# Optimization experiments

Measured on AMD Instinct MI355X. Metric: run time of the kernel, lower is better.

## Reference

```python
import math
import jax, jax.numpy as jnp
import numpy as np

B, T, D = 2, 2048, 2048
DH, NQ, NKV = 128, 16, 4
QPG = NQ // NKV  # queries per group = 4
ROPE_BASE = 10000.0
YARN_SCALE = 2.0
ORIG_MAX_LEN = 4096
BETA_FAST, BETA_SLOW = 32.0, 1.0
EPS = 1.1920929e-07  # torch.finfo(float32).eps, RMSNorm default
MSCALE = 0.1 * math.log(YARN_SCALE) + 1.0
ATTN_SCALE = 1.0 / (MSCALE * math.sqrt(DH))


def _yarn_inv_freq():
    inv_freq = 1.0 / ROPE_BASE ** (np.arange(0, DH, 2, dtype=np.float32) / DH)
    wavelengths = 2.0 * math.pi / inv_freq
    low_w = ORIG_MAX_LEN / BETA_SLOW
    high_w = ORIG_MAX_LEN / BETA_FAST
    gamma = np.clip((low_w - wavelengths) / (low_w - high_w), 0.0, 1.0)
    return (gamma * inv_freq + (1.0 - gamma) * inv_freq / YARN_SCALE).astype(np.float32)


def setup_inputs() -> dict:
    key = jax.random.key(0)
    k0, k1, k2, k3 = jax.random.split(key, 4)
    x = jax.random.normal(k0, (B, T, D), jnp.float32)
    Wq = jax.random.normal(k1, (D, DH * NQ), jnp.float32) * 0.02
    Wkv = jax.random.normal(k2, (D, 2 * DH * NKV), jnp.float32) * 0.02
    Wout = jax.random.normal(k3, (DH * NQ, D), jnp.float32) * 0.02
    q_norm_w = jnp.ones((DH,), jnp.float32)
    k_norm_w = jnp.ones((DH,), jnp.float32)
    inv_freq = jnp.asarray(_yarn_inv_freq())
    return {"x": x, "Wq": Wq, "Wkv": Wkv, "Wout": Wout,
            "q_norm_w": q_norm_w, "k_norm_w": k_norm_w, "inv_freq": inv_freq}


def _rmsnorm(x, w):
    ms = jnp.mean(jnp.square(x), axis=-1, keepdims=True)
    return x * jax.lax.rsqrt(ms + EPS) * w


def _apply_rope(x, inv_freq):
    # x: (..., T, DH)
    t = jnp.arange(x.shape[-2], dtype=inv_freq.dtype)
    freqs = jnp.outer(t, inv_freq)               # (T, DH//2)
    emb = jnp.concatenate([freqs, freqs], -1)     # (T, DH)
    cos, sin = jnp.cos(emb), jnp.sin(emb)
    half = x.shape[-1] // 2
    x_rot = jnp.concatenate([-x[..., half:], x[..., :half]], -1)
    return x * cos + x_rot * sin


def reference(x, Wq, Wkv, Wout, q_norm_w, k_norm_w, inv_freq):
    q = x @ Wq                                    # (B, T, NQ*DH)
    kv = x @ Wkv                                  # (B, T, 2*NKV*DH)
    k, v = jnp.split(kv, 2, axis=-1)              # each (B, T, NKV*DH)
    # b t (qpg g d) -> b qpg g t d
    q = q.reshape(B, T, QPG, NKV, DH).transpose(0, 2, 3, 1, 4)
    # b t (g d) -> b g t d
    k = k.reshape(B, T, NKV, DH).transpose(0, 2, 1, 3)
    v = v.reshape(B, T, NKV, DH).transpose(0, 2, 1, 3)
    q = _apply_rope(_rmsnorm(q, q_norm_w), inv_freq)
    k = _apply_rope(_rmsnorm(k, k_norm_w), inv_freq)
    scores = jnp.einsum('bqgtd,bgsd->bqgts', q, k) * ATTN_SCALE
    causal = jnp.tril(jnp.ones((T, T), bool))
    scores = jnp.where(causal, scores, -jnp.inf)
    attn = jax.nn.softmax(scores, axis=-1)
    out = jnp.einsum('bqgts,bgsd->bqgtd', attn, v)
    # b qpg g t d -> b t (qpg g d)
    out = out.transpose(0, 3, 1, 2, 4).reshape(B, T, NQ * DH)
    return out @ Wout
```

## Files before the change

kernel.cpp:

```cpp
#include <hip/hip_runtime.h>
#include <math.h>


typedef __attribute__((ext_vector_type(8))) short s16x8;
typedef __attribute__((ext_vector_type(4))) float f32x4;
typedef __attribute__((ext_vector_type(4))) unsigned int u32x4;

__device__ __forceinline__ unsigned short f2bf(float x) {
  union { float f; unsigned int u; } v; v.f = x;
  return (unsigned short)((v.u + 0x7FFFu + ((v.u >> 16) & 1u)) >> 16);
}

__device__ __forceinline__ float bf2f(unsigned short x) {
  union { unsigned int u; float f; } v; v.u = (unsigned int)x << 16;
  return v.f;
}

__device__ __forceinline__ unsigned int cvt_pk_bf16(float lo, float hi) {
  unsigned int r;
  asm("v_cvt_pk_bf16_f32 %0, %1, %2" : "=v"(r) : "v"(lo), "v"(hi));
  return r;
}

#define GLD_LDS16(g, l)                                            \
  __builtin_amdgcn_global_load_lds(                                \
      (const __attribute__((address_space(1))) void*)(g),          \
      (__attribute__((address_space(3))) void*)(l), 16, 0, 0)

__global__ __launch_bounds__(256) void cast_bf16_k(const float* __restrict__ in,
                                                   unsigned short* __restrict__ out) {
  int i = blockIdx.x * 256 + threadIdx.x;
  float4 v = ((const float4*)in)[i];
  unsigned long long pack = (unsigned long long)f2bf(v.x)
                          | ((unsigned long long)f2bf(v.y) << 16)
                          | ((unsigned long long)f2bf(v.z) << 32)
                          | ((unsigned long long)f2bf(v.w) << 48);
  ((unsigned long long*)out)[i] = pack;
}

__global__ __launch_bounds__(256) void wtrans_k(const float* __restrict__ in,
                                                unsigned short* __restrict__ out,
                                                int R, int C) {
  __shared__ unsigned short lt[64][65];
  const int r0 = blockIdx.x * 64, c0 = blockIdx.y * 64;
  const int j = threadIdx.x & 63, i4 = threadIdx.x >> 6;
#pragma unroll
  for (int p = 0; p < 16; ++p) {
    int i = p * 4 + i4;
    lt[i][j] = f2bf(in[(size_t)(r0 + i) * C + c0 + j]);
  }
  __syncthreads();
#pragma unroll
  for (int p = 0; p < 16; ++p) {
    int i = p * 4 + i4;
    out[(size_t)(c0 + i) * R + r0 + j] = lt[j][i];
  }
}

__global__ __launch_bounds__(256) void trig_k(const float* __restrict__ invf,
                                              float2* __restrict__ cstab) {
  int i = blockIdx.x * 256 + threadIdx.x;
  int t = i >> 6, f = i & 63;
  float s, c;
  sincosf((float)t * invf[f], &s, &c);
  cstab[i] = make_float2(c, s);
}

template <int OUTBF>
__global__ __launch_bounds__(256) void gemm_bt_t(const unsigned short* __restrict__ A,
                                                 const unsigned short* __restrict__ Bt,
                                                 void* __restrict__ Cv,
                                                 int M, int N, int K) {
  __shared__ alignas(16) unsigned short sA[2][128][32];
  __shared__ alignas(16) unsigned short sB[2][128][32];
  const int tid = threadIdx.x;
  const int lane = tid & 63;
  const int w = tid >> 6;
  const int wm = (w >> 1) * 64, wn = (w & 1) * 64;
  const int nwg = gridDim.x * gridDim.y;
  int bid = blockIdx.y * gridDim.x + blockIdx.x;
  bid = (bid & 7) * (nwg >> 3) + (bid >> 3);
  const int m0 = (bid % gridDim.x) * 128, n0 = (bid / gridDim.x) * 128;
  const int l15 = lane & 15, lhi = lane >> 4;
  f32x4 acc[4][4];
#pragma unroll
  for (int i = 0; i < 4; ++i)
#pragma unroll
    for (int j = 0; j < 4; ++j) acc[i][j] = (f32x4){0.f, 0.f, 0.f, 0.f};
  const int row = tid >> 2;
  const int srcslot = (tid & 3) ^ ((row >> 1) & 3);
  const unsigned short* gA0 = A + (size_t)(m0 + row) * K + srcslot * 8;
  const unsigned short* gA1 = A + (size_t)(m0 + 64 + row) * K + srcslot * 8;
  const unsigned short* gB0 = Bt + (size_t)(n0 + row) * K + srcslot * 8;
  const unsigned short* gB1 = Bt + (size_t)(n0 + 64 + row) * K + srcslot * 8;
  char* ldsA = (char*)&sA[0][0][0] + w * 1024;
  char* ldsB = (char*)&sB[0][0][0] + w * 1024;
  auto STAGE = [&](int bb, int k0) {
    GLD_LDS16(gA0 + k0, ldsA + bb * 8192);
    GLD_LDS16(gA1 + k0, ldsA + bb * 8192 + 4096);
    GLD_LDS16(gB0 + k0, ldsB + bb * 8192);
    GLD_LDS16(gB1 + k0, ldsB + bb * 8192 + 4096);
  };
  const int sphys = (lhi ^ ((l15 >> 1) & 3)) * 8;
  const int nt = K >> 5;
  STAGE(0, 0);
  __syncthreads();
  int cur = 0;
  for (int t = 0; t < nt; ++t) {
    if (t + 1 < nt) STAGE(cur ^ 1, (t + 1) * 32);
    s16x8 af[4], bfr[4];
#pragma unroll
    for (int i = 0; i < 4; ++i) af[i] = *(const s16x8*)&sA[cur][wm + i * 16 + l15][sphys];
#pragma unroll
    for (int j = 0; j < 4; ++j) bfr[j] = *(const s16x8*)&sB[cur][wn + j * 16 + l15][sphys];
#pragma unroll
    for (int i = 0; i < 4; ++i)
#pragma unroll
      for (int j = 0; j < 4; ++j)
        acc[i][j] = __builtin_amdgcn_mfma_f32_16x16x32_bf16(af[i], bfr[j], acc[i][j], 0, 0, 0);
    __syncthreads();
    cur ^= 1;
  }
  const int col0 = n0 + wn + l15;
  const int row00 = m0 + wm + lhi * 4;
  if (OUTBF) {
    unsigned short* C = (unsigned short*)Cv;
#pragma unroll
    for (int i = 0; i < 4; ++i)
#pragma unroll
      for (int j = 0; j < 4; ++j)
#pragma unroll
        for (int r = 0; r < 4; ++r)
          C[(size_t)(row00 + i * 16 + r) * N + col0 + j * 16] = f2bf(acc[i][j][r]);
  } else {
    float* C = (float*)Cv;
#pragma unroll
    for (int i = 0; i < 4; ++i)
#pragma unroll
      for (int j = 0; j < 4; ++j)
#pragma unroll
        for (int r = 0; r < 4; ++r)
          C[(size_t)(row00 + i * 16 + r) * N + col0 + j * 16] = acc[i][j][r];
  }
}

__global__ __launch_bounds__(256) void normrope_k(const unsigned short* __restrict__ qkvb,
                                                  const float* __restrict__ qw,
                                                  const float* __restrict__ kw,
                                                  const float2* __restrict__ cstab,
                                                  unsigned short* __restrict__ qT,
                                                  unsigned short* __restrict__ kT) {
  constexpr float FOLD =
      (float)(1.4426950408889634 / ((0.1 * 0.6931471805599453 + 1.0) * 11.313708498984761));
  int wid = blockIdx.x * 4 + (threadIdx.x >> 6);
  int lane = threadIdx.x & 63;
  const unsigned short* src; const float* wgt; unsigned short* dst;
  int t; float fold;
  if (wid < 65536) {
    int bt = wid >> 4, h = wid & 15;
    int b = bt >> 11; t = bt & 2047;
    src = qkvb + (size_t)bt * 3072 + h * 128;
    wgt = qw;
    dst = qT + ((size_t)(b * 16 + h) * 2048 + t) * 128;
    fold = FOLD;
  } else {
    int id = wid - 65536;
    int bt = id >> 2, g = id & 3;
    int b = bt >> 11; t = bt & 2047;
    src = qkvb + (size_t)bt * 3072 + 2048 + g * 128;
    wgt = kw;
    dst = kT + ((size_t)(b * 4 + g) * 2048 + t) * 128;
    fold = 1.0f;
  }
  unsigned int vv = ((const unsigned int*)src)[lane];
  float vx = bf2f((unsigned short)(vv & 0xffff));
  float vy = bf2f((unsigned short)(vv >> 16));
  float ss = vx * vx + vy * vy;
#pragma unroll
  for (int m = 32; m; m >>= 1) ss += __shfl_xor(ss, m);
  float rs = rsqrtf(ss * (1.0f / 128.0f) + 1.1920929e-07f);
  float2 wv = ((const float2*)wgt)[lane];
  float xn0 = vx * rs * wv.x;
  float xn1 = vy * rs * wv.y;
  float px = __shfl_xor(xn0, 32);
  float py = __shfl_xor(xn1, 32);
  float sgn = (lane < 32) ? -1.0f : 1.0f;
  int f0 = (2 * lane) & 63;
  float4 cs = ((const float4*)cstab)[((size_t)t * 64 + f0) >> 1];
  float r0 = (xn0 * cs.x + sgn * px * cs.y) * fold;
  float r1 = (xn1 * cs.z + sgn * py * cs.w) * fold;
  unsigned int packed = (unsigned int)f2bf(r0) | ((unsigned int)f2bf(r1) << 16);
  ((unsigned int*)dst)[lane] = packed;
}

__global__ __launch_bounds__(256) void vtrans_k(const unsigned short* __restrict__ qkvb,
                                                unsigned short* __restrict__ vT) {
  __shared__ unsigned short lt[64][65];
  const int tt0 = blockIdx.x * 64;
  const int dd0 = blockIdx.y * 64;
  const int b = blockIdx.z >> 2, g = blockIdx.z & 3;
  const int j = threadIdx.x & 63, i4 = threadIdx.x >> 6;
  const unsigned short* src = qkvb + (size_t)b * 2048 * 3072 + 2560 + g * 128 + dd0;
#pragma unroll
  for (int p = 0; p < 16; ++p) {
    int i = p * 4 + i4;
    lt[i][j] = src[(size_t)(tt0 + i) * 3072 + j];
  }
  __syncthreads();
  unsigned short* dst = vT + ((size_t)(b * 4 + g) * 128 + dd0) * 2048 + tt0;
  const int jp = (j & 32) | (((j & 15) >> 2) << 3) | (((j >> 4) & 1) << 2) | (j & 3);
#pragma unroll
  for (int p = 0; p < 16; ++p) {
    int d = p * 4 + i4;
    dst[(size_t)d * 2048 + jp] = lt[j][d];
  }
}

__global__ __launch_bounds__(256) void attn_k(const unsigned short* __restrict__ qT,
                                              const unsigned short* __restrict__ kT,
                                              const unsigned short* __restrict__ vT,
                                              unsigned short* __restrict__ ao) {
  __shared__ alignas(16) unsigned short sK[64][136];
  __shared__ alignas(16) unsigned short sVt[128][72];
  const int tid = threadIdx.x;
  const int lane = tid & 63;
  const int w = tid >> 6;
  const int l15 = lane & 15, lhi = lane >> 4;
  const int bid = blockIdx.x;
  const int xg = bid & 7;
  const int b = xg >> 2, g = xg & 3;
  const int hh = (bid >> 3) & 3;
  const int h = hh * 4 + g;
  const int qt = 31 - (bid >> 5);
  const int q0 = qt * 64;
  const unsigned short* Qb = qT + ((size_t)(b * 16 + h) * 2048) * 128;
  const unsigned short* Kb = kT + ((size_t)(b * 4 + g) * 2048) * 128;
  const unsigned short* Vb = vT + ((size_t)(b * 4 + g) * 128) * 2048;
  const int kr = tid >> 4, kc = (tid & 15) * 8;
  const int vr = tid >> 3, vc = (tid & 7) * 8;

  s16x8 qfr[4];
#pragma unroll
  for (int ks = 0; ks < 4; ++ks)
    qfr[ks] = *(const s16x8*)(Qb + (size_t)(q0 + w * 16 + l15) * 128 + ks * 32 + lhi * 8);

  u32x4 gk[4], gv[4];
#pragma unroll
  for (int p = 0; p < 4; ++p) {
    gk[p] = *(const u32x4*)(Kb + (size_t)(p * 16 + kr) * 128 + kc);
    gv[p] = *(const u32x4*)(Vb + (size_t)(p * 32 + vr) * 2048 + vc);
  }
  f32x4 o[8];
#pragma unroll
  for (int i = 0; i < 8; ++i) o[i] = (f32x4){0.f, 0.f, 0.f, 0.f};
  f32x4 o9 = (f32x4){0.f, 0.f, 0.f, 0.f};
  float m_run = -INFINITY;
  s16x8 ones;
#pragma unroll
  for (int j = 0; j < 8; ++j) ones[j] = (short)0x3F80;

  for (int kt = 0; kt <= qt; ++kt) {
    __syncthreads();
#pragma unroll
    for (int p = 0; p < 4; ++p) {
      *(u32x4*)&sK[p * 16 + kr][kc] = gk[p];
      *(u32x4*)&sVt[p * 32 + vr][vc] = gv[p];
    }
    __syncthreads();
    if (kt < qt) {
#pragma unroll
      for (int p = 0; p < 4; ++p) {
        gk[p] = *(const u32x4*)(Kb + (size_t)((kt + 1) * 64 + p * 16 + kr) * 128 + kc);
        gv[p] = *(const u32x4*)(Vb + (size_t)(p * 32 + vr) * 2048 + (kt + 1) * 64 + vc);
      }
    }
    f32x4 s[4];
#pragma unroll
    for (int jn = 0; jn < 4; ++jn) s[jn] = (f32x4){0.f, 0.f, 0.f, 0.f};
#pragma unroll
    for (int ks = 0; ks < 4; ++ks)
#pragma unroll
      for (int jn = 0; jn < 4; ++jn) {
        s16x8 ak = *(const s16x8*)&sK[jn * 16 + l15][ks * 32 + lhi * 8];
        s[jn] = __builtin_amdgcn_mfma_f32_16x16x32_bf16(ak, qfr[ks], s[jn], 0, 0, 0);
      }
    if (kt == qt) {
#pragma unroll
      for (int jn = 0; jn < 4; ++jn)
#pragma unroll
        for (int r = 0; r < 4; ++r)
          if (jn * 16 + lhi * 4 + r > w * 16 + l15) s[jn][r] = -INFINITY;
    }
    float mx = fmaxf(fmaxf(fmaxf(s[0][0], s[0][1]), fmaxf(s[0][2], s[0][3])),
                     fmaxf(fmaxf(s[1][0], s[1][1]), fmaxf(s[1][2], s[1][3])));
    mx = fmaxf(mx, fmaxf(fmaxf(fmaxf(s[2][0], s[2][1]), fmaxf(s[2][2], s[2][3])),
                         fmaxf(fmaxf(s[3][0], s[3][1]), fmaxf(s[3][2], s[3][3]))));
    mx = fmaxf(mx, __shfl_xor(mx, 16));
    mx = fmaxf(mx, __shfl_xor(mx, 32));
    if (!__all(mx - m_run <= 8.0f)) {
      float mnew = fmaxf(m_run, mx);
      float scale = exp2f(m_run - mnew);
      m_run = mnew;
      float sc_o[4];
#pragma unroll
      for (int r = 0; r < 4; ++r) sc_o[r] = __shfl(scale, lhi * 4 + r);
#pragma unroll
      for (int nt = 0; nt < 8; ++nt)
#pragma unroll
        for (int r = 0; r < 4; ++r) o[nt][r] *= sc_o[r];
#pragma unroll
      for (int r = 0; r < 4; ++r) o9[r] *= sc_o[r];
    }
    float pp[4][4];
#pragma unroll
    for (int jn = 0; jn < 4; ++jn)
#pragma unroll
      for (int r = 0; r < 4; ++r) pp[jn][r] = exp2f(s[jn][r] - m_run);
    union { s16x8 v; unsigned int d[4]; } pa0, pa1;
#pragma unroll
    for (int d = 0; d < 2; ++d) {
      pa0.d[d]     = cvt_pk_bf16(pp[0][2 * d], pp[0][2 * d + 1]);
      pa0.d[2 + d] = cvt_pk_bf16(pp[1][2 * d], pp[1][2 * d + 1]);
      pa1.d[d]     = cvt_pk_bf16(pp[2][2 * d], pp[2][2 * d + 1]);
      pa1.d[2 + d] = cvt_pk_bf16(pp[3][2 * d], pp[3][2 * d + 1]);
    }
    o9 = __builtin_amdgcn_mfma_f32_16x16x32_bf16(pa0.v, ones, o9, 0, 0, 0);
    o9 = __builtin_amdgcn_mfma_f32_16x16x32_bf16(pa1.v, ones, o9, 0, 0, 0);
#pragma unroll
    for (int nt = 0; nt < 8; ++nt) {
      s16x8 vb0 = *(const s16x8*)&sVt[nt * 16 + l15][lhi * 8];
      o[nt] = __builtin_amdgcn_mfma_f32_16x16x32_bf16(pa0.v, vb0, o[nt], 0, 0, 0);
    }
#pragma unroll
    for (int nt = 0; nt < 8; ++nt) {
      s16x8 vb1 = *(const s16x8*)&sVt[nt * 16 + l15][32 + lhi * 8];
      o[nt] = __builtin_amdgcn_mfma_f32_16x16x32_bf16(pa1.v, vb1, o[nt], 0, 0, 0);
    }
  }
#pragma unroll
  for (int r = 0; r < 4; ++r) {
    float invr = 1.0f / o9[r];
    int t = q0 + w * 16 + lhi * 4 + r;
    size_t base = ((size_t)b * 2048 + t) * 2048 + h * 128;
#pragma unroll
    for (int nt = 0; nt < 8; ++nt)
      ao[base + nt * 16 + l15] = f2bf(o[nt][r] * invr);
  }
}

extern "C" void kernel_launch(void* const* d_in, const int* in_sizes, int n_in,
                              void* d_out, int out_size, void* d_ws, size_t ws_size,
                              hipStream_t stream) {
  (void)in_sizes; (void)n_in; (void)out_size; (void)ws_size;
  const float* x    = (const float*)d_in[0];
  const float* Wq   = (const float*)d_in[1];
  const float* Wkv  = (const float*)d_in[2];
  const float* Wout = (const float*)d_in[3];
  const float* qw   = (const float*)d_in[4];
  const float* kw   = (const float*)d_in[5];
  const float* invf = (const float*)d_in[6];
  float* out = (float*)d_out;

  char* ws = (char*)d_ws;
  size_t off = 0;
  auto alloc = [&](size_t bytes) -> void* {
    void* p = ws + off; off += (bytes + 255) & ~(size_t)255; return p;
  };
  unsigned short* xb    = (unsigned short*)alloc((size_t)4096 * 2048 * 2);
  unsigned short* wqkvt = (unsigned short*)alloc((size_t)3072 * 2048 * 2);
  unsigned short* wot   = (unsigned short*)alloc((size_t)2048 * 2048 * 2);
  unsigned short* qkvb  = (unsigned short*)alloc((size_t)4096 * 3072 * 2);
  float2* cstab = (float2*)alloc((size_t)2048 * 64 * 8);
  unsigned short* qT = (unsigned short*)alloc((size_t)2 * 16 * 2048 * 128 * 2);
  unsigned short* kT = (unsigned short*)alloc((size_t)2 * 4 * 2048 * 128 * 2);
  unsigned short* vT = (unsigned short*)alloc((size_t)2 * 4 * 128 * 2048 * 2);
  unsigned short* ao = (unsigned short*)alloc((size_t)4096 * 2048 * 2);

  cast_bf16_k<<<8192, 256, 0, stream>>>(x, xb);
  wtrans_k<<<dim3(32, 32), 256, 0, stream>>>(Wq, wqkvt, 2048, 2048);
  wtrans_k<<<dim3(32, 16), 256, 0, stream>>>(Wkv, wqkvt + (size_t)2048 * 2048, 2048, 1024);
  wtrans_k<<<dim3(32, 32), 256, 0, stream>>>(Wout, wot, 2048, 2048);
  trig_k<<<512, 256, 0, stream>>>(invf, cstab);
  gemm_bt_t<1><<<dim3(32, 24), 256, 0, stream>>>(xb, wqkvt, qkvb, 4096, 3072, 2048);
  normrope_k<<<20480, 256, 0, stream>>>(qkvb, qw, kw, cstab, qT, kT);
  vtrans_k<<<dim3(32, 2, 8), 256, 0, stream>>>(qkvb, vT);
  attn_k<<<1024, 256, 0, stream>>>(qT, kT, vT, ao);
  gemm_bt_t<0><<<dim3(32, 16), 256, 0, stream>>>(ao, wot, out, 4096, 2048, 2048);
}
```

Baseline: 222.0 us.

## Use 128x256 tiles with 512 threads and triple-buffered async LDS pipeline in GEMMs

Both projection GEMMs now use a 128x256 output tile computed by 8 waves, with a three-stage LDS ring filled by direct global-to-LDS loads. A vmcnt wait plus a single barrier per K step replaces the two syncthreads, and loads run two stages ahead. MFMA issue is wrapped in raised wave priority. This aims to hide global-load latency and reuse each A tile across twice as many columns, at the cost of more LDS per block and fewer blocks in the grid.

```diff
diff --git a/kernel.cpp b/kernel.cpp
--- a/kernel.cpp
+++ b/kernel.cpp
@@ -67,62 +67,66 @@
 }
 
 template <int OUTBF>
-__global__ __launch_bounds__(256) void gemm_bt_t(const unsigned short* __restrict__ A,
-                                                 const unsigned short* __restrict__ Bt,
-                                                 void* __restrict__ Cv,
-                                                 int M, int N, int K) {
-  __shared__ alignas(16) unsigned short sA[2][128][32];
-  __shared__ alignas(16) unsigned short sB[2][128][32];
+__global__ __launch_bounds__(512) void gemm_bt2_t(const unsigned short* __restrict__ A,
+                                                  const unsigned short* __restrict__ Bt,
+                                                  void* __restrict__ Cv,
+                                                  int M, int N, int K) {
+  __shared__ alignas(16) unsigned short sA[3][128][32];
+  __shared__ alignas(16) unsigned short sB[3][256][32];
   const int tid = threadIdx.x;
   const int lane = tid & 63;
   const int w = tid >> 6;
-  const int wm = (w >> 1) * 64, wn = (w & 1) * 64;
+  const int wm2 = w >> 2, wn4 = w & 3;
+  const int l15 = lane & 15, lhi = lane >> 4;
   const int nwg = gridDim.x * gridDim.y;
   int bid = blockIdx.y * gridDim.x + blockIdx.x;
   bid = (bid & 7) * (nwg >> 3) + (bid >> 3);
-  const int m0 = (bid % gridDim.x) * 128, n0 = (bid / gridDim.x) * 128;
-  const int l15 = lane & 15, lhi = lane >> 4;
+  const int m0 = (bid % gridDim.x) * 128, n0 = (bid / gridDim.x) * 256;
   f32x4 acc[4][4];
 #pragma unroll
   for (int i = 0; i < 4; ++i)
 #pragma unroll
     for (int j = 0; j < 4; ++j) acc[i][j] = (f32x4){0.f, 0.f, 0.f, 0.f};
   const int row = tid >> 2;
-  const int srcslot = (tid & 3) ^ ((row >> 1) & 3);
-  const unsigned short* gA0 = A + (size_t)(m0 + row) * K + srcslot * 8;
-  const unsigned short* gA1 = A + (size_t)(m0 + 64 + row) * K + srcslot * 8;
+  const int srcslot = (tid & 3) ^ ((tid >> 3) & 3);
+  const unsigned short* gA  = A  + (size_t)(m0 + row) * K + srcslot * 8;
   const unsigned short* gB0 = Bt + (size_t)(n0 + row) * K + srcslot * 8;
-  const unsigned short* gB1 = Bt + (size_t)(n0 + 64 + row) * K + srcslot * 8;
+  const unsigned short* gB1 = Bt + (size_t)(n0 + 128 + row) * K + srcslot * 8;
   char* ldsA = (char*)&sA[0][0][0] + w * 1024;
   char* ldsB = (char*)&sB[0][0][0] + w * 1024;
   auto STAGE = [&](int bb, int k0) {
-    GLD_LDS16(gA0 + k0, ldsA + bb * 8192);
-    GLD_LDS16(gA1 + k0, ldsA + bb * 8192 + 4096);
-    GLD_LDS16(gB0 + k0, ldsB + bb * 8192);
-    GLD_LDS16(gB1 + k0, ldsB + bb * 8192 + 4096);
+    GLD_LDS16(gA + k0, ldsA + bb * 8192);
+    GLD_LDS16(gB0 + k0, ldsB + bb * 16384);
+    GLD_LDS16(gB1 + k0, ldsB + bb * 16384 + 8192);
   };
   const int sphys = (lhi ^ ((l15 >> 1) & 3)) * 8;
   const int nt = K >> 5;
   STAGE(0, 0);
-  __syncthreads();
-  int cur = 0;
+  STAGE(1, 32);
   for (int t = 0; t < nt; ++t) {
-    if (t + 1 < nt) STAGE(cur ^ 1, (t + 1) * 32);
-    s16x8 af[4], bfr[4];
-#pragma unroll
-    for (int i = 0; i < 4; ++i) af[i] = *(const s16x8*)&sA[cur][wm + i * 16 + l15][sphys];
-#pragma unroll
-    for (int j = 0; j < 4; ++j) bfr[j] = *(const s16x8*)&sB[cur][wn + j * 16 + l15][sphys];
+    if (t < nt - 1) asm volatile("s_waitcnt vmcnt(3)" ::: "memory");
+    else            asm volatile("s_waitcnt vmcnt(0)" ::: "memory");
+    __builtin_amdgcn_s_barrier();
+    asm volatile("" ::: "memory");
+    if (t + 2 < nt) STAGE((t + 2) % 3, (t + 2) * 32);
+    const int cb = t % 3;
+    s16x8 af[4], bf[4];
 #pragma unroll
     for (int i = 0; i < 4; ++i)
+      af[i] = *(const s16x8*)&sA[cb][wm2 * 64 + i * 16 + l15][sphys];
+#pragma unroll
+    for (int j = 0; j < 4; ++j)
+      bf[j] = *(const s16x8*)&sB[cb][wn4 * 64 + j * 16 + l15][sphys];
+    __builtin_amdgcn_s_setprio(1);
+#pragma unroll
+    for (int i = 0; i < 4; ++i)
 #pragma unroll
       for (int j = 0; j < 4; ++j)
-        acc[i][j] = __builtin_amdgcn_mfma_f32_16x16x32_bf16(af[i], bfr[j], acc[i][j], 0, 0, 0);
-    __syncthreads();
-    cur ^= 1;
-  }
-  const int col0 = n0 + wn + l15;
-  const int row00 = m0 + wm + lhi * 4;
+        acc[i][j] = __builtin_amdgcn_mfma_f32_16x16x32_bf16(af[i], bf[j], acc[i][j], 0, 0, 0);
+    __builtin_amdgcn_s_setprio(0);
+  }
+  const int col0 = n0 + wn4 * 64 + l15;
+  const int row00 = m0 + wm2 * 64 + lhi * 4;
   if (OUTBF) {
     unsigned short* C = (unsigned short*)Cv;
 #pragma unroll
@@ -381,9 +385,9 @@
   wtrans_k<<<dim3(32, 16), 256, 0, stream>>>(Wkv, wqkvt + (size_t)2048 * 2048, 2048, 1024);
   wtrans_k<<<dim3(32, 32), 256, 0, stream>>>(Wout, wot, 2048, 2048);
   trig_k<<<512, 256, 0, stream>>>(invf, cstab);
-  gemm_bt_t<1><<<dim3(32, 24), 256, 0, stream>>>(xb, wqkvt, qkvb, 4096, 3072, 2048);
+  gemm_bt2_t<1><<<dim3(32, 12), 512, 0, stream>>>(xb, wqkvt, qkvb, 4096, 3072, 2048);
   normrope_k<<<20480, 256, 0, stream>>>(qkvb, qw, kw, cstab, qT, kT);
   vtrans_k<<<dim3(32, 2, 8), 256, 0, stream>>>(qkvb, vT);
   attn_k<<<1024, 256, 0, stream>>>(qT, kT, vT, ao);
-  gemm_bt_t<0><<<dim3(32, 16), 256, 0, stream>>>(ao, wot, out, 4096, 2048, 2048);
-}
+  gemm_bt2_t<0><<<dim3(32, 8), 512, 0, stream>>>(ao, wot, out, 4096, 2048, 2048);
+}
```

Result: slower. 250.4 us (+12.8%).
